# Kernel optimization log

Measured on AMD Instinct MI355X. Metric: run time of the kernel, lower is better.

## Reference

```python
import jax, jax.numpy as jnp
import numpy as np
from jax import lax

NUM_LABELS = 64  # groundtruth labels in [0, 64); label 0 = background (ignored in pair counts)


def _edges(H, W):
    # channel 0: edge (i,j)-(i+1,j); channel 1: edge (i,j)-(i,j+1)
    idx = np.arange(H * W).reshape(H, W)
    u0 = idx.copy(); v0 = np.roll(idx, -1, axis=0)
    u0[-1, :] = 0; v0[-1, :] = 0  # invalid boundary edges -> self edge, no-op
    u1 = idx.copy(); v1 = np.roll(idx, -1, axis=1)
    u1[:, -1] = 0; v1[:, -1] = 0
    u = np.concatenate([u0.ravel(), u1.ravel()]).astype(np.int32)
    v = np.concatenate([v0.ravel(), v1.ravel()]).astype(np.int32)
    return jnp.asarray(u), jnp.asarray(v)


def _find(parent, x, iters):
    # union-by-size keeps tree depth <= log2(N)+1, so a fixed number of hops suffices
    return lax.fori_loop(0, iters, lambda i, p: parent[p], x)


def _npairs(order, u, v, labels, pos):
    """Kruskal over edges sorted by descending affinity; for each merging edge,
    count pairs of voxels for which it is the maximin edge (pos: same nonzero
    label; neg: different nonzero labels). Pure int computation (non-diff)."""
    N = labels.shape[0]
    iters = int(np.ceil(np.log2(N))) + 2
    parent0 = jnp.arange(N, dtype=jnp.int32)
    size0 = jnp.ones(N, jnp.int32)
    counts0 = jax.nn.one_hot(labels, NUM_LABELS, dtype=jnp.int32)  # [N, L] label histogram per root

    def step(carry, e):
        parent, size, counts = carry
        ru = _find(parent, u[e], iters)
        rv = _find(parent, v[e], iters)
        cu = counts[ru]; cv = counts[rv]
        same = jnp.dot(cu[1:], cv[1:])          # same-nonzero-label pairs
        tu = cu[1:].sum(); tv = cv[1:].sum()    # nonzero-label voxel counts
        n = same if pos else tu * tv - same     # differing-label pairs for neg pass
        merge = ru != rv
        n = jnp.where(merge, n, 0)
        big = jnp.where(size[ru] >= size[rv], ru, rv)
        small = ru + rv - big
        parent = parent.at[small].set(jnp.where(merge, big, parent[small]))
        size = size.at[big].add(jnp.where(merge, size[small], 0))
        counts = counts.at[big].add(jnp.where(merge, counts[small], 0))
        return (parent, size, counts), n

    _, n = lax.scan(step, (parent0, size0, counts0), order)
    return n  # [E] int32, aligned with sorted order


def _malis_grad(aff, labels, u, v):
    # aff [E] float, labels [N] int. MALIS pseudo-loss gradients:
    # pos pass grad_e = n_pos_e * (a_e - 1); neg pass grad_e = n_neg_e * a_e;
    # combined = -(pos + neg) / 2 (as in MalisLoss.forward).
    order = jnp.argsort(-lax.stop_gradient(aff)).astype(jnp.int32)
    a_sorted = aff[order]
    n_pos = _npairs(order, u, v, labels, True).astype(aff.dtype)
    n_neg = _npairs(order, u, v, labels, False).astype(aff.dtype)
    g_sorted = n_pos * (a_sorted - 1.0) + n_neg * a_sorted
    return jnp.zeros_like(aff).at[order].set(-0.5 * g_sorted)


def setup_inputs() -> dict:
    key = jax.random.key(0)
    k1, k2 = jax.random.split(key)
    affinities = jax.random.uniform(k1, (2, 2, 128, 128), dtype=jnp.float32)
    groundtruth = jax.random.randint(k2, (2, 128, 128), 0, NUM_LABELS, dtype=jnp.int64)
    return {"affinities": affinities, "groundtruth": groundtruth}


def reference(affinities, groundtruth):
    B, C, H, W = affinities.shape
    u, v = _edges(H, W)
    aff = affinities.reshape(B, C * H * W)
    lab = groundtruth.reshape(B, H * W).astype(jnp.int32)
    grads = jax.vmap(lambda a, l: _malis_grad(a, l, u, v))(aff, lab)
    return grads.sum()  # pseudo_loss
```

## Files before the change

### kernel.cpp

```cpp
#include <hip/hip_runtime.h>

#define HDIM 128
#define WDIM 128
#define NPIX (HDIM * WDIM)
#define NEDGE (2 * NPIX)
#define BANDS 256
#define MAXK 256

typedef unsigned long long ull;

__device__ __forceinline__ void decode_edge(unsigned e, int& u, int& v) {
  if (e >= (unsigned)NEDGE) { u = 0; v = 0; return; }
  if (e < NPIX) {
    if (e < NPIX - WDIM) { u = (int)e; v = (int)e + WDIM; } else { u = 0; v = 0; }
  } else {
    unsigned t2 = e - NPIX;
    if ((t2 & (WDIM - 1)) != (WDIM - 1)) { u = (int)t2; v = (int)t2 + 1; } else { u = 0; v = 0; }
  }
}

__device__ __forceinline__ int bucket_of(float a) {
  int f = (int)(a * 256.0f);
  f = f < 0 ? 0 : (f > 255 ? 255 : f);
  return 255 - f;
}


__global__ __launch_bounds__(1024) void hist_kernel(const float* __restrict__ aff_g,
                                                    unsigned* __restrict__ ghist) {
  __shared__ unsigned h[BANDS];
  const int img = blockIdx.x >> 5;
  const int slice = blockIdx.x & 31;
  const int tid = threadIdx.x;
  if (tid < BANDS) h[tid] = 0;
  __syncthreads();
  const unsigned e = (unsigned)(slice * 1024 + tid);
  const float a = aff_g[(size_t)img * NEDGE + e];
  int u, v; decode_edge(e, u, v);
  if (u != v) atomicAdd(&h[bucket_of(a)], 1u);
  __syncthreads();
  if (tid < BANDS && h[tid]) atomicAdd(&ghist[img * BANDS + tid], h[tid]);
}

__global__ __launch_bounds__(1024) void scatter_kernel(const float* __restrict__ aff_g,
                                                       const unsigned* __restrict__ ghist,
                                                       unsigned* __restrict__ gcur,
                                                       unsigned* __restrict__ gbase,
                                                       ull* __restrict__ keys_g,
                                                       unsigned* __restrict__ uv_g,
                                                       float* __restrict__ out, int out_n) {
  __shared__ unsigned hb[BANDS];
  __shared__ unsigned lh[BANDS];
  __shared__ unsigned go[BANDS];
  const int img = blockIdx.x >> 5;
  const int slice = blockIdx.x & 31;
  const int tid = threadIdx.x;
  if (blockIdx.x == 0 && tid < out_n) out[tid] = 0.f;
  if (tid < BANDS) { hb[tid] = ghist[img * BANDS + tid]; lh[tid] = 0; }
  __syncthreads();
  for (int off = 1; off < BANDS; off <<= 1) {
    unsigned vv = 0;
    if (tid < BANDS && tid >= off) vv = hb[tid - off];
    __syncthreads();
    if (tid < BANDS) hb[tid] += vv;
    __syncthreads();
  }
  const unsigned e = (unsigned)(slice * 1024 + tid);
  const float a = aff_g[(size_t)img * NEDGE + e];
  int u, v; decode_edge(e, u, v);
  int b = -1; unsigned lpos = 0;
  if (u != v) { b = bucket_of(a); lpos = atomicAdd(&lh[b], 1u); }
  __syncthreads();
  if (tid < BANDS && lh[tid]) go[tid] = atomicAdd(&gcur[img * BANDS + tid], lh[tid]);
  if (slice == 0) {
    if (tid < BANDS) gbase[img * (BANDS + 1) + tid] = (tid == 0) ? 0u : hb[tid - 1];
    if (tid == 0) gbase[img * (BANDS + 1) + BANDS] = hb[BANDS - 1];
  }
  __syncthreads();
  if (b >= 0) {
    const unsigned base = (b == 0) ? 0u : hb[b - 1];
    const unsigned pos = base + go[b] + lpos;
    unsigned bits = __float_as_uint(a);
    unsigned ob = (bits & 0x80000000u) ? ~bits : (bits | 0x80000000u);
    keys_g[(size_t)img * NEDGE + pos] = ((ull)(~ob) << 32) | e;
    uv_g[(size_t)img * NEDGE + pos] = ((unsigned)u << 16) | (unsigned)v;
  }
}

__device__ __forceinline__ int cc_find(volatile unsigned* p, int x) {
  int px = (int)p[x];
  while (px != x) {
    int g = (int)p[px];
    if (g != px) p[x] = (unsigned)g;
    x = px; px = g;
  }
  return x;
}

__device__ __forceinline__ void uf_find2(unsigned* pn, int x, int y,
                                         int& rx, int& ry,
                                         unsigned& nzx, unsigned& nzy) {
  unsigned wx = pn[x];
  unsigned wy = pn[y];
  while (true) {
    int px = (int)(wx & 0xFFFFu);
    int py = (int)(wy & 0xFFFFu);
    bool mx = (px != x);
    bool my = (py != y);
    if (!mx && !my) break;
    if (mx) {
      unsigned wpx = pn[px];
      int gx = (int)(wpx & 0xFFFFu);
      if (gx != px) { pn[x] = (wx & 0xFFFF0000u) | (unsigned)gx; x = gx; wx = pn[gx]; }
      else { x = px; wx = wpx; }
    }
    if (my) {
      unsigned wpy = pn[py];
      int gy = (int)(wpy & 0xFFFFu);
      if (gy != py) { pn[y] = (wy & 0xFFFF0000u) | (unsigned)gy; y = gy; wy = pn[gy]; }
      else { y = py; wy = wpy; }
    }
  }
  rx = x; ry = y; nzx = wx >> 16; nzy = wy >> 16;
}

__device__ __forceinline__ ull shflx64(ull x, int m) {
  int lo = __shfl_xor((int)(unsigned)x, m, 64);
  int hi = __shfl_xor((int)(unsigned)(x >> 32), m, 64);
  return ((ull)(unsigned)hi << 32) | (unsigned)lo;
}

__global__ __launch_bounds__(1024) void band_kernel(const int* __restrict__ gt,
                                                    const ull* __restrict__ keys_g,
                                                    const unsigned* __restrict__ uv_g,
                                                    const unsigned* __restrict__ gbase,
                                                    float* __restrict__ out) {
  __shared__ unsigned pn[NPIX];
  __shared__ ull skbuf[MAXK];
  const int img = blockIdx.x / BANDS;
  const int braw = blockIdx.x % BANDS;
  const int band = (img & 1) ? (BANDS - 1 - braw) : braw;
  const int* lab = gt + (size_t)img * NPIX;
  const ull* keys = keys_g + (size_t)img * NEDGE;
  const unsigned* uvp = uv_g + (size_t)img * NEDGE;
  const int tid = threadIdx.x;
  const unsigned bstart = gbase[img * (BANDS + 1) + band];
  const unsigned bend   = gbase[img * (BANDS + 1) + band + 1];
  unsigned cnt = bend - bstart; if (cnt > MAXK) cnt = MAXK;

  if (band == 0) {
    if (tid < 64) pn[tid] = 0;
    __syncthreads();
    for (int i = tid; i < NPIX; i += 1024) atomicAdd(&pn[(unsigned)lab[i] & 63u], 1u);
    __syncthreads();
    if (tid == 0) {
      double s = 0.0;
      for (int l = 1; l < 64; ++l) { double m = (double)pn[l]; s += m * (m - 1.0) * 0.5; }
      atomicAdd(out, (float)(0.5 * s));
    }
    __syncthreads();
  }

  for (int i = tid; i < NPIX / 4; i += 1024) {
    uint4 w; w.x = 4u * i; w.y = 4u * i + 1u; w.z = 4u * i + 2u; w.w = 4u * i + 3u;
    ((uint4*)pn)[i] = w;
  }
  if (tid < (int)cnt) skbuf[tid] = keys[bstart + tid];
  __syncthreads();

  volatile unsigned* vp = pn;
  for (unsigned i = tid; i < bstart; i += 1024) {
    const unsigned p = uvp[i];
    int u = (int)(p >> 16), v = (int)(p & 0xFFFFu);
    while (true) {
      int ru = cc_find(vp, u), rv = cc_find(vp, v);
      if (ru == rv) break;
      if (ru < rv) { int t = ru; ru = rv; rv = t; }
      unsigned old = atomicCAS(&pn[ru], (unsigned)ru, (unsigned)rv);
      if (old == (unsigned)ru) break;
      u = ru; v = rv;
    }
  }
  __syncthreads();

  ull myv[4];
  if (tid < 64) {
    const int lane = tid;
#pragma unroll
    for (int r = 0; r < 4; ++r) {
      unsigned idx = (unsigned)(r * 64 + lane);
      myv[r] = (idx < cnt) ? skbuf[idx] : ~0ull;
    }
#pragma unroll
    for (unsigned k = 2; k <= 256; k <<= 1) {
#pragma unroll
      for (unsigned j = k >> 1; j; j >>= 1) {
        if (j >= 64) {
          const int rj = (int)(j >> 6);
#pragma unroll
          for (int r = 0; r < 4; ++r) {
            if (!(r & rj)) {
              const int p = r | rj;
              const bool dir = ((((unsigned)r << 6) & k) == 0);
              ull a0 = myv[r], a1 = myv[p];
              if ((a0 > a1) == dir) { myv[r] = a1; myv[p] = a0; }
            }
          }
        } else {
#pragma unroll
          for (int r = 0; r < 4; ++r) {
            ull pv = shflx64(myv[r], (int)j);
            const bool low = ((lane & (int)j) == 0);
            const bool dir = (((((unsigned)r << 6) | (unsigned)lane) & k) == 0);
            const bool takemin = (low == dir);
            const bool less = (myv[r] < pv);
            myv[r] = (less == takemin) ? myv[r] : pv;
          }
        }
      }
    }
  } else {
    const int t = tid - 64;
    int prev = -1; unsigned acc = 0; bool multi = false;
    for (int k = 0; k < 18; ++k) {
      int i = t + k * 960;
      if (i >= NPIX) break;
      int r = i; unsigned p;
      while (((p = vp[r]) & 0xFFFFu) != (unsigned)r) r = (int)(p & 0xFFFFu);
      if (i != r) pn[i] = (unsigned)r;
      unsigned c = (lab[i] != 0) ? 1u : 0u;
      if (r != prev) {
        if (prev >= 0) { if (acc) atomicAdd(&pn[prev], acc << 16); multi = true; }
        prev = r; acc = c;
      } else {
        acc += c;
      }
    }
    const int wl = tid & 63;
    int first = __shfl(prev, 0);
    bool uni = __all(!multi && prev == first);
    if (uni) {
      unsigned s = acc;
      for (int off = 32; off; off >>= 1) s += __shfl_down(s, off);
      if (wl == 0 && s) atomicAdd(&pn[prev], s << 16);
    } else if (acc) {
      atomicAdd(&pn[prev], acc << 16);
    }
  }
  __syncthreads();

  if (tid < 64) {
    const int lane = tid;
    double acc = 0.0;
#pragma unroll
    for (int b8 = 0; b8 < 4; ++b8) {
      if ((unsigned)(b8 * 64) >= cnt) break;
      const ull myk_b = myv[b8];
      unsigned e = (unsigned)myk_b;
      unsigned khi = (unsigned)(myk_b >> 32);
      int u, v; decode_edge(e, u, v);
      const bool valid = (u != v);
      unsigned ob = ~khi;
      unsigned bits = (ob & 0x80000000u) ? (ob & 0x7FFFFFFFu) : ~ob;
      const float a = __uint_as_float(bits);

      int ru, rv; unsigned nzu, nzv;
      uf_find2(pn, u, v, ru, rv, nzu, nzv);

      unsigned long long m = __ballot(valid && (ru != rv));
      int myW = 0, myL = 0; unsigned snap = 0;
      while (m) {
        const int j = (int)(__ffsll(m) - 1);
        m &= m - 1;
        const int ruj = __builtin_amdgcn_readlane(ru, j);
        const int rvj = __builtin_amdgcn_readlane(rv, j);
        const unsigned nzuj = (unsigned)__builtin_amdgcn_readlane((int)nzu, j);
        const unsigned nzvj = (unsigned)__builtin_amdgcn_readlane((int)nzv, j);
        const bool live = (ruj != rvj);
        const unsigned mnz = nzuj + nzvj;
        int W = (nzuj >= nzvj) ? ruj : rvj;
        int L = ruj + rvj - W;
        W = live ? W : -1;
        L = live ? L : -1;
        const int sj = live ? j : 64;
        const unsigned spk = nzuj | (nzvj << 16);
        const bool turn = (lane == sj);
        if (turn) { myW = W; myL = L; snap = spk; }
        const bool uW = (ru == W), uL = (ru == L);
        const bool vW = (rv == W), vL = (rv == L);
        if (uL) ru = W;
        if (uW | uL) nzu = mnz;
        if (vL) rv = W;
        if (vW | vL) nzv = mnz;
      }
      pn[u] = (unsigned)ru;
      pn[v] = (unsigned)rv;
      if (myW != myL) {
        pn[myL] = (unsigned)myW;
        acc += (double)((snap & 0xFFFFu) * (snap >> 16)) * (double)a;
      }
      pn[ru] = (nzu << 16) | (unsigned)ru;
      pn[rv] = (nzv << 16) | (unsigned)rv;
    }
    for (int off = 32; off > 0; off >>= 1) acc += __shfl_down(acc, off);
    if (lane == 0) atomicAdd(out, (float)(-0.5 * acc));
  }
}

extern "C" void kernel_launch(void* const* d_in, const int* in_sizes, int n_in,
                              void* d_out, int out_size, void* d_ws, size_t ws_size,
                              hipStream_t stream) {
  const float* aff = (const float*)d_in[0];
  const int* gt = (const int*)d_in[1];
  float* out = (float*)d_out;
  const int B = in_sizes[1] / NPIX;

  ull* keys = (ull*)d_ws;
  unsigned* uvp = (unsigned*)(keys + (size_t)B * NEDGE);
  unsigned* ghist = uvp + (size_t)B * NEDGE;
  unsigned* gcur = ghist + (size_t)B * BANDS;
  unsigned* gbase = gcur + (size_t)B * BANDS;

  hipMemsetAsync(ghist, 0, sizeof(unsigned) * 2 * (size_t)B * BANDS, stream);
  hist_kernel<<<dim3(B * 32), dim3(1024), 0, stream>>>(aff, ghist);
  scatter_kernel<<<dim3(B * 32), dim3(1024), 0, stream>>>(aff, ghist, gcur, gbase,
                                                          keys, uvp, out, out_size);
  band_kernel<<<dim3(B * BANDS), dim3(1024), 0, stream>>>(gt, keys, uvp, gbase, out);
}
```

Baseline: 120.6 us.

## Precompute union-find checkpoints so band blocks replay only edges since checkpoint

Adds a checkpoint kernel that builds the connected-component state after every 32 bands (7 snapshots per image) and writes flattened root arrays to workspace. Each band block now loads the nearest snapshot and replays only the edges between that checkpoint and its band start, instead of all preceding edges from scratch. This removes most of the redundant prefix union-find work across the 256 band blocks, at the cost of an extra serialized kernel launch. It also adds snapshot reads of 64 KB per block.

Measured after the change: 145.5 us. 20.6% more time.

```diff
diff --git a/kernel.cpp b/kernel.cpp
--- a/kernel.cpp
+++ b/kernel.cpp
@@ -6,6 +6,7 @@
 #define NEDGE (2 * NPIX)
 #define BANDS 256
 #define MAXK 256
+#define NCP 7
 
 typedef unsigned long long ull;
 
@@ -95,6 +96,17 @@
     x = px; px = g;
   }
   return x;
+}
+
+__device__ __forceinline__ void cc_hook(volatile unsigned* vp, unsigned* pn, int u, int v) {
+  while (true) {
+    int ru = cc_find(vp, u), rv = cc_find(vp, v);
+    if (ru == rv) break;
+    if (ru < rv) { int t = ru; ru = rv; rv = t; }
+    unsigned old = atomicCAS(&pn[ru], (unsigned)ru, (unsigned)rv);
+    if (old == (unsigned)ru) break;
+    u = ru; v = rv;
+  }
 }
 
 __device__ __forceinline__ void uf_find2(unsigned* pn, int x, int y,
@@ -130,10 +142,40 @@
   return ((ull)(unsigned)hi << 32) | (unsigned)lo;
 }
 
+__global__ __launch_bounds__(1024) void cp_kernel(const unsigned* __restrict__ uv_g,
+                                                  const unsigned* __restrict__ gbase,
+                                                  unsigned* __restrict__ snap_g) {
+  __shared__ unsigned pn[NPIX];
+  const int img = blockIdx.x / NCP;
+  const int c = blockIdx.x % NCP + 1;
+  const unsigned* uvp = uv_g + (size_t)img * NEDGE;
+  const unsigned end = gbase[img * (BANDS + 1) + 32 * c];
+  unsigned* snap = snap_g + ((size_t)img * NCP + (c - 1)) * NPIX;
+  const int tid = threadIdx.x;
+
+  for (int i = tid; i < NPIX / 4; i += 1024) {
+    uint4 w; w.x = 4u * i; w.y = 4u * i + 1u; w.z = 4u * i + 2u; w.w = 4u * i + 3u;
+    ((uint4*)pn)[i] = w;
+  }
+  __syncthreads();
+  volatile unsigned* vp = pn;
+  for (unsigned i = tid; i < end; i += 1024) {
+    const unsigned p = uvp[i];
+    cc_hook(vp, pn, (int)(p >> 16), (int)(p & 0xFFFFu));
+  }
+  __syncthreads();
+  for (int i = tid; i < NPIX; i += 1024) {
+    int r = i; unsigned p;
+    while ((p = vp[r]) != (unsigned)r) r = (int)p;
+    snap[i] = (unsigned)r;
+  }
+}
+
 __global__ __launch_bounds__(1024) void band_kernel(const int* __restrict__ gt,
                                                     const ull* __restrict__ keys_g,
                                                     const unsigned* __restrict__ uv_g,
                                                     const unsigned* __restrict__ gbase,
+                                                    const unsigned* __restrict__ snap_g,
                                                     float* __restrict__ out) {
   __shared__ unsigned pn[NPIX];
   __shared__ ull skbuf[MAXK];
@@ -161,25 +203,26 @@
     __syncthreads();
   }
 
-  for (int i = tid; i < NPIX / 4; i += 1024) {
-    uint4 w; w.x = 4u * i; w.y = 4u * i + 1u; w.z = 4u * i + 2u; w.w = 4u * i + 3u;
-    ((uint4*)pn)[i] = w;
+  const int cbase = band & ~31;
+  unsigned cstart = 0;
+  if (cbase == 0) {
+    for (int i = tid; i < NPIX / 4; i += 1024) {
+      uint4 w; w.x = 4u * i; w.y = 4u * i + 1u; w.z = 4u * i + 2u; w.w = 4u * i + 3u;
+      ((uint4*)pn)[i] = w;
+    }
+  } else {
+    const unsigned* snap = snap_g + ((size_t)img * NCP + (band >> 5) - 1) * NPIX;
+    for (int i = tid; i < NPIX / 4; i += 1024)
+      ((uint4*)pn)[i] = ((const uint4*)snap)[i];
+    cstart = gbase[img * (BANDS + 1) + cbase];
   }
   if (tid < (int)cnt) skbuf[tid] = keys[bstart + tid];
   __syncthreads();
 
   volatile unsigned* vp = pn;
-  for (unsigned i = tid; i < bstart; i += 1024) {
+  for (unsigned i = cstart + tid; i < bstart; i += 1024) {
     const unsigned p = uvp[i];
-    int u = (int)(p >> 16), v = (int)(p & 0xFFFFu);
-    while (true) {
-      int ru = cc_find(vp, u), rv = cc_find(vp, v);
-      if (ru == rv) break;
-      if (ru < rv) { int t = ru; ru = rv; rv = t; }
-      unsigned old = atomicCAS(&pn[ru], (unsigned)ru, (unsigned)rv);
-      if (old == (unsigned)ru) break;
-      u = ru; v = rv;
-    }
+    cc_hook(vp, pn, (int)(p >> 16), (int)(p & 0xFFFFu));
   }
   __syncthreads();
 
@@ -320,10 +363,12 @@
   unsigned* ghist = uvp + (size_t)B * NEDGE;
   unsigned* gcur = ghist + (size_t)B * BANDS;
   unsigned* gbase = gcur + (size_t)B * BANDS;
+  unsigned* snaps = gbase + (size_t)B * (BANDS + 1);
 
   hipMemsetAsync(ghist, 0, sizeof(unsigned) * 2 * (size_t)B * BANDS, stream);
   hist_kernel<<<dim3(B * 32), dim3(1024), 0, stream>>>(aff, ghist);
   scatter_kernel<<<dim3(B * 32), dim3(1024), 0, stream>>>(aff, ghist, gcur, gbase,
                                                           keys, uvp, out, out_size);
-  band_kernel<<<dim3(B * BANDS), dim3(1024), 0, stream>>>(gt, keys, uvp, gbase, out);
-}
+  cp_kernel<<<dim3(B * NCP), dim3(1024), 0, stream>>>(uvp, gbase, snaps);
+  band_kernel<<<dim3(B * BANDS), dim3(1024), 0, stream>>>(gt, keys, uvp, gbase, snaps, out);
+}
```

## Group consecutive bands into variable-size ranges per workgroup to cut redundant prefix rebuilds

Applied to the files above, without the earlier changes.

Instead of one workgroup per band, each workgroup now processes a contiguous range of bands whose width shrinks as the start band grows (range_step). After rebuilding the connected components of all edges before the range start, it runs the sorted per-band Kruskal step sequentially across the range, reusing the union-find state between bands. This removes most of the repeated prefix union-find rebuilds and per-block shared-memory initialisation, which scale with the band count. The cost is fewer workgroups, less parallelism, and serial per-band work with barriers inside each workgroup. The range sizing is meant to balance prefix length against the number of bands per range.

Result: slower. 180.0 us (+49.2%).

```diff
diff --git a/kernel.cpp b/kernel.cpp
--- a/kernel.cpp
+++ b/kernel.cpp
@@ -23,6 +23,11 @@
   int f = (int)(a * 256.0f);
   f = f < 0 ? 0 : (f > 255 ? 255 : f);
   return 255 - f;
+}
+
+__host__ __device__ __forceinline__ int range_step(int s) {
+  int K = (2112 - 7 * s) / 320;
+  return K < 1 ? 1 : K;
 }
 
 
@@ -95,6 +100,17 @@
     x = px; px = g;
   }
   return x;
+}
+
+__device__ __forceinline__ void cc_hook(volatile unsigned* vp, unsigned* pn, int u, int v) {
+  while (true) {
+    int ru = cc_find(vp, u), rv = cc_find(vp, v);
+    if (ru == rv) break;
+    if (ru < rv) { int t = ru; ru = rv; rv = t; }
+    unsigned old = atomicCAS(&pn[ru], (unsigned)ru, (unsigned)rv);
+    if (old == (unsigned)ru) break;
+    u = ru; v = rv;
+  }
 }
 
 __device__ __forceinline__ void uf_find2(unsigned* pn, int x, int y,
@@ -130,33 +146,33 @@
   return ((ull)(unsigned)hi << 32) | (unsigned)lo;
 }
 
-__global__ __launch_bounds__(1024) void band_kernel(const int* __restrict__ gt,
-                                                    const ull* __restrict__ keys_g,
-                                                    const unsigned* __restrict__ uv_g,
-                                                    const unsigned* __restrict__ gbase,
-                                                    float* __restrict__ out) {
+__global__ __launch_bounds__(1024) void range_kernel(const int* __restrict__ gt,
+                                                     const ull* __restrict__ keys_g,
+                                                     const unsigned* __restrict__ uv_g,
+                                                     const unsigned* __restrict__ gbase,
+                                                     float* __restrict__ out, int NR) {
   __shared__ unsigned pn[NPIX];
   __shared__ ull skbuf[MAXK];
-  const int img = blockIdx.x / BANDS;
-  const int braw = blockIdx.x % BANDS;
-  const int band = (img & 1) ? (BANDS - 1 - braw) : braw;
+  const int img = blockIdx.x / NR;
+  const int rid = blockIdx.x % NR;
+  int s = 0;
+  for (int j = 0; j < rid; ++j) s += range_step(s);
+  int e = s + range_step(s); if (e > BANDS) e = BANDS;
   const int* lab = gt + (size_t)img * NPIX;
   const ull* keys = keys_g + (size_t)img * NEDGE;
   const unsigned* uvp = uv_g + (size_t)img * NEDGE;
+  const unsigned* base = gbase + img * (BANDS + 1);
   const int tid = threadIdx.x;
-  const unsigned bstart = gbase[img * (BANDS + 1) + band];
-  const unsigned bend   = gbase[img * (BANDS + 1) + band + 1];
-  unsigned cnt = bend - bstart; if (cnt > MAXK) cnt = MAXK;
-
-  if (band == 0) {
+
+  if (s == 0) {
     if (tid < 64) pn[tid] = 0;
     __syncthreads();
     for (int i = tid; i < NPIX; i += 1024) atomicAdd(&pn[(unsigned)lab[i] & 63u], 1u);
     __syncthreads();
     if (tid == 0) {
-      double s = 0.0;
-      for (int l = 1; l < 64; ++l) { double m = (double)pn[l]; s += m * (m - 1.0) * 0.5; }
-      atomicAdd(out, (float)(0.5 * s));
+      double h = 0.0;
+      for (int l = 1; l < 64; ++l) { double m = (double)pn[l]; h += m * (m - 1.0) * 0.5; }
+      atomicAdd(out, (float)(0.5 * h));
     }
     __syncthreads();
   }
@@ -165,66 +181,20 @@
     uint4 w; w.x = 4u * i; w.y = 4u * i + 1u; w.z = 4u * i + 2u; w.w = 4u * i + 3u;
     ((uint4*)pn)[i] = w;
   }
-  if (tid < (int)cnt) skbuf[tid] = keys[bstart + tid];
   __syncthreads();
 
   volatile unsigned* vp = pn;
-  for (unsigned i = tid; i < bstart; i += 1024) {
+  const unsigned pstart = base[s];
+  for (unsigned i = tid; i < pstart; i += 1024) {
     const unsigned p = uvp[i];
-    int u = (int)(p >> 16), v = (int)(p & 0xFFFFu);
-    while (true) {
-      int ru = cc_find(vp, u), rv = cc_find(vp, v);
-      if (ru == rv) break;
-      if (ru < rv) { int t = ru; ru = rv; rv = t; }
-      unsigned old = atomicCAS(&pn[ru], (unsigned)ru, (unsigned)rv);
-      if (old == (unsigned)ru) break;
-      u = ru; v = rv;
-    }
-  }
-  __syncthreads();
-
-  ull myv[4];
-  if (tid < 64) {
-    const int lane = tid;
-#pragma unroll
-    for (int r = 0; r < 4; ++r) {
-      unsigned idx = (unsigned)(r * 64 + lane);
-      myv[r] = (idx < cnt) ? skbuf[idx] : ~0ull;
-    }
-#pragma unroll
-    for (unsigned k = 2; k <= 256; k <<= 1) {
-#pragma unroll
-      for (unsigned j = k >> 1; j; j >>= 1) {
-        if (j >= 64) {
-          const int rj = (int)(j >> 6);
-#pragma unroll
-          for (int r = 0; r < 4; ++r) {
-            if (!(r & rj)) {
-              const int p = r | rj;
-              const bool dir = ((((unsigned)r << 6) & k) == 0);
-              ull a0 = myv[r], a1 = myv[p];
-              if ((a0 > a1) == dir) { myv[r] = a1; myv[p] = a0; }
-            }
-          }
-        } else {
-#pragma unroll
-          for (int r = 0; r < 4; ++r) {
-            ull pv = shflx64(myv[r], (int)j);
-            const bool low = ((lane & (int)j) == 0);
-            const bool dir = (((((unsigned)r << 6) | (unsigned)lane) & k) == 0);
-            const bool takemin = (low == dir);
-            const bool less = (myv[r] < pv);
-            myv[r] = (less == takemin) ? myv[r] : pv;
-          }
-        }
-      }
-    }
-  } else {
-    const int t = tid - 64;
+    cc_hook(vp, pn, (int)(p >> 16), (int)(p & 0xFFFFu));
+  }
+  __syncthreads();
+
+  {
     int prev = -1; unsigned acc = 0; bool multi = false;
-    for (int k = 0; k < 18; ++k) {
-      int i = t + k * 960;
-      if (i >= NPIX) break;
+    for (int k = 0; k < 16; ++k) {
+      int i = tid + k * 1024;
       int r = i; unsigned p;
       while (((p = vp[r]) & 0xFFFFu) != (unsigned)r) r = (int)(p & 0xFFFFu);
       if (i != r) pn[i] = (unsigned)r;
@@ -240,70 +210,116 @@
     int first = __shfl(prev, 0);
     bool uni = __all(!multi && prev == first);
     if (uni) {
-      unsigned s = acc;
-      for (int off = 32; off; off >>= 1) s += __shfl_down(s, off);
-      if (wl == 0 && s) atomicAdd(&pn[prev], s << 16);
+      unsigned m = acc;
+      for (int off = 32; off; off >>= 1) m += __shfl_down(m, off);
+      if (wl == 0 && m) atomicAdd(&pn[prev], m << 16);
     } else if (acc) {
       atomicAdd(&pn[prev], acc << 16);
     }
   }
   __syncthreads();
 
+  double accWG = 0.0;
+  for (int band = s; band < e; ++band) {
+    const unsigned bstart = base[band];
+    unsigned cnt = base[band + 1] - bstart; if (cnt > MAXK) cnt = MAXK;
+    if (tid < (int)cnt) skbuf[tid] = keys[bstart + tid];
+    __syncthreads();
+
+    if (tid < 64) {
+      const int lane = tid;
+      ull myv[4];
+#pragma unroll
+      for (int r = 0; r < 4; ++r) {
+        unsigned idx = (unsigned)(r * 64 + lane);
+        myv[r] = (idx < cnt) ? skbuf[idx] : ~0ull;
+      }
+#pragma unroll
+      for (unsigned k = 2; k <= 256; k <<= 1) {
+#pragma unroll
+        for (unsigned j = k >> 1; j; j >>= 1) {
+          if (j >= 64) {
+            const int rj = (int)(j >> 6);
+#pragma unroll
+            for (int r = 0; r < 4; ++r) {
+              if (!(r & rj)) {
+                const int p = r | rj;
+                const bool dir = ((((unsigned)r << 6) & k) == 0);
+                ull a0 = myv[r], a1 = myv[p];
+                if ((a0 > a1) == dir) { myv[r] = a1; myv[p] = a0; }
+              }
+            }
+          } else {
+#pragma unroll
+            for (int r = 0; r < 4; ++r) {
+              ull pv = shflx64(myv[r], (int)j);
+              const bool low = ((lane & (int)j) == 0);
+              const bool dir = (((((unsigned)r << 6) | (unsigned)lane) & k) == 0);
+              const bool takemin = (low == dir);
+              const bool less = (myv[r] < pv);
+              myv[r] = (less == takemin) ? myv[r] : pv;
+            }
+          }
+        }
+      }
+
+#pragma unroll
+      for (int b8 = 0; b8 < 4; ++b8) {
+        if ((unsigned)(b8 * 64) >= cnt) break;
+        const ull myk_b = myv[b8];
+        unsigned ei = (unsigned)myk_b;
+        unsigned khi = (unsigned)(myk_b >> 32);
+        int u, v; decode_edge(ei, u, v);
+        const bool valid = (u != v);
+        unsigned ob = ~khi;
+        unsigned bits = (ob & 0x80000000u) ? (ob & 0x7FFFFFFFu) : ~ob;
+        const float a = __uint_as_float(bits);
+
+        int ru, rv; unsigned nzu, nzv;
+        uf_find2(pn, u, v, ru, rv, nzu, nzv);
+
+        unsigned long long m = __ballot(valid && (ru != rv));
+        int myW = 0, myL = 0; unsigned snap = 0;
+        while (m) {
+          const int j = (int)(__ffsll(m) - 1);
+          m &= m - 1;
+          const int ruj = __builtin_amdgcn_readlane(ru, j);
+          const int rvj = __builtin_amdgcn_readlane(rv, j);
+          const unsigned nzuj = (unsigned)__builtin_amdgcn_readlane((int)nzu, j);
+          const unsigned nzvj = (unsigned)__builtin_amdgcn_readlane((int)nzv, j);
+          const bool live = (ruj != rvj);
+          const unsigned mnz = nzuj + nzvj;
+          int W = (nzuj >= nzvj) ? ruj : rvj;
+          int L = ruj + rvj - W;
+          W = live ? W : -1;
+          L = live ? L : -1;
+          const int sj = live ? j : 64;
+          const unsigned spk = nzuj | (nzvj << 16);
+          const bool turn = (lane == sj);
+          if (turn) { myW = W; myL = L; snap = spk; }
+          const bool uW = (ru == W), uL = (ru == L);
+          const bool vW = (rv == W), vL = (rv == L);
+          if (uL) ru = W;
+          if (uW | uL) nzu = mnz;
+          if (vL) rv = W;
+          if (vW | vL) nzv = mnz;
+        }
+        pn[u] = (unsigned)ru;
+        pn[v] = (unsigned)rv;
+        if (myW != myL) {
+          pn[myL] = (unsigned)myW;
+          accWG += (double)((snap & 0xFFFFu) * (snap >> 16)) * (double)a;
+        }
+        pn[ru] = (nzu << 16) | (unsigned)ru;
+        pn[rv] = (nzv << 16) | (unsigned)rv;
+      }
+    }
+    __syncthreads();
+  }
+
   if (tid < 64) {
-    const int lane = tid;
-    double acc = 0.0;
-#pragma unroll
-    for (int b8 = 0; b8 < 4; ++b8) {
-      if ((unsigned)(b8 * 64) >= cnt) break;
-      const ull myk_b = myv[b8];
-      unsigned e = (unsigned)myk_b;
-      unsigned khi = (unsigned)(myk_b >> 32);
-      int u, v; decode_edge(e, u, v);
-      const bool valid = (u != v);
-      unsigned ob = ~khi;
-      unsigned bits = (ob & 0x80000000u) ? (ob & 0x7FFFFFFFu) : ~ob;
-      const float a = __uint_as_float(bits);
-
-      int ru, rv; unsigned nzu, nzv;
-      uf_find2(pn, u, v, ru, rv, nzu, nzv);
-
-      unsigned long long m = __ballot(valid && (ru != rv));
-      int myW = 0, myL = 0; unsigned snap = 0;
-      while (m) {
-        const int j = (int)(__ffsll(m) - 1);
-        m &= m - 1;
-        const int ruj = __builtin_amdgcn_readlane(ru, j);
-        const int rvj = __builtin_amdgcn_readlane(rv, j);
-        const unsigned nzuj = (unsigned)__builtin_amdgcn_readlane((int)nzu, j);
-        const unsigned nzvj = (unsigned)__builtin_amdgcn_readlane((int)nzv, j);
-        const bool live = (ruj != rvj);
-        const unsigned mnz = nzuj + nzvj;
-        int W = (nzuj >= nzvj) ? ruj : rvj;
-        int L = ruj + rvj - W;
-        W = live ? W : -1;
-        L = live ? L : -1;
-        const int sj = live ? j : 64;
-        const unsigned spk = nzuj | (nzvj << 16);
-        const bool turn = (lane == sj);
-        if (turn) { myW = W; myL = L; snap = spk; }
-        const bool uW = (ru == W), uL = (ru == L);
-        const bool vW = (rv == W), vL = (rv == L);
-        if (uL) ru = W;
-        if (uW | uL) nzu = mnz;
-        if (vL) rv = W;
-        if (vW | vL) nzv = mnz;
-      }
-      pn[u] = (unsigned)ru;
-      pn[v] = (unsigned)rv;
-      if (myW != myL) {
-        pn[myL] = (unsigned)myW;
-        acc += (double)((snap & 0xFFFFu) * (snap >> 16)) * (double)a;
-      }
-      pn[ru] = (nzu << 16) | (unsigned)ru;
-      pn[rv] = (nzv << 16) | (unsigned)rv;
-    }
-    for (int off = 32; off > 0; off >>= 1) acc += __shfl_down(acc, off);
-    if (lane == 0) atomicAdd(out, (float)(-0.5 * acc));
+    for (int off = 32; off > 0; off >>= 1) accWG += __shfl_down(accWG, off);
+    if (tid == 0) atomicAdd(out, (float)(-0.5 * accWG));
   }
 }
 
@@ -321,9 +337,12 @@
   unsigned* gcur = ghist + (size_t)B * BANDS;
   unsigned* gbase = gcur + (size_t)B * BANDS;
 
+  int NR = 0;
+  for (int s = 0; s < BANDS; ++NR) s += range_step(s);
+
   hipMemsetAsync(ghist, 0, sizeof(unsigned) * 2 * (size_t)B * BANDS, stream);
   hist_kernel<<<dim3(B * 32), dim3(1024), 0, stream>>>(aff, ghist);
   scatter_kernel<<<dim3(B * 32), dim3(1024), 0, stream>>>(aff, ghist, gcur, gbase,
                                                           keys, uvp, out, out_size);
-  band_kernel<<<dim3(B * BANDS), dim3(1024), 0, stream>>>(gt, keys, uvp, gbase, out);
-}
+  range_kernel<<<dim3(B * NR), dim3(1024), 0, stream>>>(gt, keys, uvp, gbase, out, NR);
+}
```

## Merge independent Kruskal edges concurrently via hashed root-ownership marks

Applied to the files above, without the earlier changes.

The per-wavefront serial loop, which broadcast each live edge with readlane and applied merges one at a time, is replaced by round-based parallel merging. In each round every live lane claims its two roots in a 2048-entry hashed mark table with atomicMin. Lanes that own both roots merge at once, while the rest re-find their roots and retry. Because the lowest lane always wins each root, sorted-order semantics are kept, and the sequential chain of up to 64 dependent iterations becomes a few rounds. The cost is extra LDS atomics, hash-collision serialization and a small extra shared buffer. The prefix-union hook is also moved into a helper function.

Result: slower. 127.2 us (+5.4%).

```diff
diff --git a/kernel.cpp b/kernel.cpp
--- a/kernel.cpp
+++ b/kernel.cpp
@@ -6,6 +6,7 @@
 #define NEDGE (2 * NPIX)
 #define BANDS 256
 #define MAXK 256
+#define MMSK 2047
 
 typedef unsigned long long ull;
 
@@ -95,6 +96,17 @@
     x = px; px = g;
   }
   return x;
+}
+
+__device__ __forceinline__ void cc_hook(volatile unsigned* vp, unsigned* pn, int u, int v) {
+  while (true) {
+    int ru = cc_find(vp, u), rv = cc_find(vp, v);
+    if (ru == rv) break;
+    if (ru < rv) { int t = ru; ru = rv; rv = t; }
+    unsigned old = atomicCAS(&pn[ru], (unsigned)ru, (unsigned)rv);
+    if (old == (unsigned)ru) break;
+    u = ru; v = rv;
+  }
 }
 
 __device__ __forceinline__ void uf_find2(unsigned* pn, int x, int y,
@@ -124,6 +136,12 @@
   rx = x; ry = y; nzx = wx >> 16; nzy = wy >> 16;
 }
 
+__device__ __forceinline__ void find1(unsigned* pn, int x, int& r, unsigned& nz) {
+  unsigned w = pn[x];
+  while ((int)(w & 0xFFFFu) != x) { x = (int)(w & 0xFFFFu); w = pn[x]; }
+  r = x; nz = w >> 16;
+}
+
 __device__ __forceinline__ ull shflx64(ull x, int m) {
   int lo = __shfl_xor((int)(unsigned)x, m, 64);
   int hi = __shfl_xor((int)(unsigned)(x >> 32), m, 64);
@@ -137,6 +155,7 @@
                                                     float* __restrict__ out) {
   __shared__ unsigned pn[NPIX];
   __shared__ ull skbuf[MAXK];
+  __shared__ unsigned mark[MMSK + 1];
   const int img = blockIdx.x / BANDS;
   const int braw = blockIdx.x % BANDS;
   const int band = (img & 1) ? (BANDS - 1 - braw) : braw;
@@ -148,6 +167,8 @@
   const unsigned bend   = gbase[img * (BANDS + 1) + band + 1];
   unsigned cnt = bend - bstart; if (cnt > MAXK) cnt = MAXK;
 
+  for (int i = tid; i <= MMSK; i += 1024) mark[i] = 0xFFFFFFFFu;
+
   if (band == 0) {
     if (tid < 64) pn[tid] = 0;
     __syncthreads();
@@ -171,15 +192,7 @@
   volatile unsigned* vp = pn;
   for (unsigned i = tid; i < bstart; i += 1024) {
     const unsigned p = uvp[i];
-    int u = (int)(p >> 16), v = (int)(p & 0xFFFFu);
-    while (true) {
-      int ru = cc_find(vp, u), rv = cc_find(vp, v);
-      if (ru == rv) break;
-      if (ru < rv) { int t = ru; ru = rv; rv = t; }
-      unsigned old = atomicCAS(&pn[ru], (unsigned)ru, (unsigned)rv);
-      if (old == (unsigned)ru) break;
-      u = ru; v = rv;
-    }
+    cc_hook(vp, pn, (int)(p >> 16), (int)(p & 0xFFFFu));
   }
   __syncthreads();
 
@@ -256,9 +269,9 @@
     for (int b8 = 0; b8 < 4; ++b8) {
       if ((unsigned)(b8 * 64) >= cnt) break;
       const ull myk_b = myv[b8];
-      unsigned e = (unsigned)myk_b;
+      unsigned ei = (unsigned)myk_b;
       unsigned khi = (unsigned)(myk_b >> 32);
-      int u, v; decode_edge(e, u, v);
+      int u, v; decode_edge(ei, u, v);
       const bool valid = (u != v);
       unsigned ob = ~khi;
       unsigned bits = (ob & 0x80000000u) ? (ob & 0x7FFFFFFFu) : ~ob;
@@ -266,41 +279,39 @@
 
       int ru, rv; unsigned nzu, nzv;
       uf_find2(pn, u, v, ru, rv, nzu, nzv);
-
-      unsigned long long m = __ballot(valid && (ru != rv));
-      int myW = 0, myL = 0; unsigned snap = 0;
+      bool live = valid && (ru != rv);
+      unsigned long long m = __ballot(live);
       while (m) {
-        const int j = (int)(__ffsll(m) - 1);
-        m &= m - 1;
-        const int ruj = __builtin_amdgcn_readlane(ru, j);
-        const int rvj = __builtin_amdgcn_readlane(rv, j);
-        const unsigned nzuj = (unsigned)__builtin_amdgcn_readlane((int)nzu, j);
-        const unsigned nzvj = (unsigned)__builtin_amdgcn_readlane((int)nzv, j);
-        const bool live = (ruj != rvj);
-        const unsigned mnz = nzuj + nzvj;
-        int W = (nzuj >= nzvj) ? ruj : rvj;
-        int L = ruj + rvj - W;
-        W = live ? W : -1;
-        L = live ? L : -1;
-        const int sj = live ? j : 64;
-        const unsigned spk = nzuj | (nzvj << 16);
-        const bool turn = (lane == sj);
-        if (turn) { myW = W; myL = L; snap = spk; }
-        const bool uW = (ru == W), uL = (ru == L);
-        const bool vW = (rv == W), vL = (rv == L);
-        if (uL) ru = W;
-        if (uW | uL) nzu = mnz;
-        if (vL) rv = W;
-        if (vW | vL) nzv = mnz;
+        unsigned h1 = 0, h2 = 0;
+        if (live) {
+          h1 = (unsigned)ru & MMSK; h2 = (unsigned)rv & MMSK;
+          atomicMin(&mark[h1], (unsigned)lane);
+          atomicMin(&mark[h2], (unsigned)lane);
+        }
+        bool indep = false;
+        if (live) indep = (mark[h1] == (unsigned)lane) && (mark[h2] == (unsigned)lane);
+        if (indep) {
+          const int W = (nzu >= nzv) ? ru : rv;
+          const int L = ru + rv - W;
+          const unsigned mnz = nzu + nzv;
+          pn[L] = (unsigned)W;
+          pn[W] = (mnz << 16) | (unsigned)W;
+          acc += (double)(nzu * nzv) * (double)a;
+          ru = W; rv = W; nzu = nzv = mnz;
+          live = false;
+        }
+        if (m & (1ull << lane)) { mark[h1] = 0xFFFFFFFFu; mark[h2] = 0xFFFFFFFFu; }
+        if (live) {
+          find1(pn, ru, ru, nzu);
+          find1(pn, rv, rv, nzv);
+          live = (ru != rv);
+        }
+        m = __ballot(live);
       }
-      pn[u] = (unsigned)ru;
-      pn[v] = (unsigned)rv;
-      if (myW != myL) {
-        pn[myL] = (unsigned)myW;
-        acc += (double)((snap & 0xFFFFu) * (snap >> 16)) * (double)a;
+      if (valid) {
+        if (u != ru) pn[u] = (unsigned)ru;
+        if (v != rv) pn[v] = (unsigned)rv;
       }
-      pn[ru] = (nzu << 16) | (unsigned)ru;
-      pn[rv] = (nzv << 16) | (unsigned)rv;
     }
     for (int off = 32; off > 0; off >>= 1) acc += __shfl_down(acc, off);
     if (lane == 0) atomicAdd(out, (float)(-0.5 * acc));
```
